# Kernel optimization log

Hardware: AMD Instinct MI355X
Metric: run time of the kernel (lower is better)

## Reference

```python
import jax, jax.numpy as jnp
import numpy as np

SOW_INIT = 1e-10  # sum_of_weights_initial_value
EPS = 1e-8       # torch.nn.CosineSimilarity default eps


def setup_inputs() -> dict:
    key = jax.random.key(0)
    k1, k2, k3 = jax.random.split(key, 3)
    input_image = jax.random.normal(k1, (1, 3, 224, 224), dtype=jnp.float32)
    masks = jax.random.uniform(k2, (1000, 224, 224), dtype=jnp.float32)
    # Linear encoder: flattened image [3*224*224] -> feature dim 128
    W = jax.random.normal(k3, (3, 224, 224, 128), dtype=jnp.float32) * 0.01
    return {"input_image": input_image, "masks": masks, "W": W}


def reference(input_image, masks, W):
    img = input_image[0]  # [3, H, W]
    # Encoder applied to (img * mask): rep_n = sum_chw (img*mask)[c,h,w] * W[c,h,w,f]
    # Precompute A[h,w,f] = sum_c img[c,h,w] * W[c,h,w,f] so masked reps never
    # materialize the [N,3,H,W] masked-image tensor.
    A = jnp.einsum('chw,chwf->hwf', img, W)          # [H, W, F]
    rep0 = jnp.sum(A, axis=(0, 1))                   # unmasked representation [F]
    reps = jnp.einsum('nhw,hwf->nf', masks, A)       # masked representations [N, F]

    # Cosine similarity (dim=1), clamped norms as in torch
    n0 = jnp.maximum(jnp.linalg.norm(rep0), EPS)
    nr = jnp.maximum(jnp.linalg.norm(reps, axis=1), EPS)
    sims = (reps @ rep0) / (nr * n0)                 # [N]

    H, Wd = masks.shape[1], masks.shape[2]
    imp0 = jnp.zeros((H, Wd), dtype=jnp.float32)
    unc0 = jnp.zeros((H, Wd), dtype=jnp.float32)
    sow0 = jnp.full((H, Wd), SOW_INIT, dtype=jnp.float32)

    def step(carry, inp):
        imp, unc, sow = carry
        m, s = inp  # mask [H,W], similarity scalar
        sow = sow + m
        prev = imp
        imp = imp + m * (s - imp) / sow
        unc = unc + (s - imp) * (s - prev) * m
        return (imp, unc, sow), None

    (imp, unc, sow), _ = jax.lax.scan(step, (imp0, unc0, sow0), (masks, sims))
    return jnp.stack([imp, unc, sow])  # [3, H, W]
```

## Files before the change

### kernel.cpp

```cpp
#include <hip/hip_runtime.h>
#include <hip/hip_bf16.h>
#include <stdint.h>

#define HWN 50176
#define NM  1000
#define FD  128
#define NSPLIT 98
#define KSTEPS 16
#define NSCAN 20
#define NPB 50

typedef __attribute__((ext_vector_type(8))) short short8;
typedef __attribute__((ext_vector_type(4))) float f32x4;

__device__ __forceinline__ unsigned short f2bf(float x) {
    union { float f; unsigned u; } v; v.f = x;
    unsigned r = v.u + 0x7FFFu + ((v.u >> 16) & 1u);
    return (unsigned short)(r >> 16);
}

#define AS1(p) ((const __attribute__((address_space(1))) unsigned int*)(p))
#define AS3(p) ((__attribute__((address_space(3))) unsigned int*)(p))

__global__ __launch_bounds__(256) void k_encode(const float* __restrict__ img,
                                                const float* __restrict__ Wt,
                                                unsigned short* __restrict__ Bpack,
                                                float* __restrict__ rep0part)
{
    const int t = threadIdx.x;
    const int f = t & 127;
    const int kt = blockIdx.x * 2 + (t >> 7);
    const int hw0 = kt * 32;
    float vals[32];
    float rsum = 0.f;
#pragma unroll
    for (int e = 0; e < 32; ++e) {
        const int hw = hw0 + e;
        float a = img[hw] * Wt[(size_t)hw * FD + f];
        a = fmaf(img[HWN + hw],     Wt[(size_t)(HWN + hw) * FD + f], a);
        a = fmaf(img[2 * HWN + hw], Wt[(size_t)(2 * HWN + hw) * FD + f], a);
        vals[e] = a;
        rsum += a;
    }
    char* tile = (char*)Bpack + (size_t)kt * 8192;
#pragma unroll
    for (int j = 0; j < 4; ++j) {
        short8 pk;
#pragma unroll
        for (int e = 0; e < 8; ++e) pk[e] = (short)f2bf(vals[j * 8 + e]);
        *reinterpret_cast<short8*>(tile + j * 2048 + (((f + j) & 127) << 4)) = pk;
    }
    __shared__ float red[256];
    red[t] = rsum;
    __syncthreads();
    if (t < 128) rep0part[(size_t)blockIdx.x * 128 + f] = red[t] + red[t + 128];
}

__global__ __launch_bounds__(256) void k_rep0red(const float* __restrict__ rep0part,
                                                 float* __restrict__ rep0)
{
    const int f = blockIdx.x;
    float s = 0.f;
    for (int b = threadIdx.x; b < 784; b += 256) s += rep0part[(size_t)b * 128 + f];
    __shared__ float red[256];
    red[threadIdx.x] = s;
    __syncthreads();
    for (int o = 128; o > 0; o >>= 1) {
        if (threadIdx.x < o) red[threadIdx.x] += red[threadIdx.x + o];
        __syncthreads();
    }
    if (threadIdx.x == 0) rep0[f] = red[0];
}

__global__ __launch_bounds__(512, 4) void k_gemm(const float* __restrict__ masks,
                                                 const unsigned short* __restrict__ Bpack,
                                                 float* __restrict__ partial)
{
    __shared__ __align__(16) char lds[3][24576];

    const int t = threadIdx.x;
    const int wv = t >> 6, lane = t & 63;
    const int lrow = lane & 15, kg = lane >> 4;
    const int mtile = blockIdx.x, split = blockIdx.y;
    const int n0 = mtile * 128;

    const int r0s = t >> 3, r1s = 64 + (t >> 3);
    const int c0 = (t & 7) ^ (r0s & 7);
    int arow0 = n0 + r0s; if (arow0 >= NM) arow0 = NM - 1;
    int arow1 = n0 + r1s; if (arow1 >= NM) arow1 = NM - 1;
    const float* aSrc0 = masks + (size_t)arow0 * HWN + split * 512 + c0 * 4;
    const float* aSrc1 = masks + (size_t)arow1 * HWN + split * 512 + c0 * 4;
    const char*  bSrc  = (const char*)Bpack + (size_t)split * (KSTEPS * 8192) + t * 16;

    const int r = wv * 16 + lrow;
    const int ao0 = r * 128 + (((2 * kg)     ^ (r & 7)) << 4);
    const int ao1 = r * 128 + ((((2 * kg)+1) ^ (r & 7)) << 4);
    int bo[8];
#pragma unroll
    for (int ft = 0; ft < 8; ++ft)
        bo[ft] = 16384 + kg * 2048 + (((ft * 16 + lrow + kg) & 127) << 4);

    f32x4 acc[8];
#pragma unroll
    for (int i = 0; i < 8; ++i) acc[i] = f32x4{0.f, 0.f, 0.f, 0.f};

#define STAGE(KS, BUF) do {                                                                              \
        char* b_ = &lds[BUF][0];                                                                         \
        __builtin_amdgcn_global_load_lds(AS1(aSrc0 + (KS) * 32), AS3(b_ + t * 16), 16, 0, 0);            \
        __builtin_amdgcn_global_load_lds(AS1(aSrc1 + (KS) * 32), AS3(b_ + 8192 + t * 16), 16, 0, 0);     \
        __builtin_amdgcn_global_load_lds(AS1(bSrc + (size_t)(KS) * 8192), AS3(b_ + 16384 + t * 16), 16, 0, 0); \
    } while (0)

    STAGE(0, 0);
    STAGE(1, 1);
    asm volatile("s_waitcnt vmcnt(3)" ::: "memory");
    __builtin_amdgcn_s_barrier();
    __builtin_amdgcn_sched_barrier(0);

    int cur = 0, stg = 2;
    for (int ks = 0; ks < KSTEPS; ++ks) {
        if (ks + 2 < KSTEPS) STAGE(ks + 2, stg);

        const char* A = &lds[cur][0];
        const f32x4 alo = *reinterpret_cast<const f32x4*>(A + ao0);
        const f32x4 ahi = *reinterpret_cast<const f32x4*>(A + ao1);
        union { short8 s; __hip_bfloat162 h[4]; } apk;
        apk.h[0] = __float22bfloat162_rn(float2{alo[0], alo[1]});
        apk.h[1] = __float22bfloat162_rn(float2{alo[2], alo[3]});
        apk.h[2] = __float22bfloat162_rn(float2{ahi[0], ahi[1]});
        apk.h[3] = __float22bfloat162_rn(float2{ahi[2], ahi[3]});
        short8 bfv[8];
#pragma unroll
        for (int ft = 0; ft < 8; ++ft)
            bfv[ft] = *reinterpret_cast<const short8*>(A + bo[ft]);

        asm volatile("s_waitcnt lgkmcnt(0)" ::: "memory");
        __builtin_amdgcn_sched_barrier(0);
        __builtin_amdgcn_s_setprio(1);
#pragma unroll
        for (int ft = 0; ft < 8; ++ft)
            acc[ft] = __builtin_amdgcn_mfma_f32_16x16x32_bf16(apk.s, bfv[ft], acc[ft], 0, 0, 0);
        __builtin_amdgcn_s_setprio(0);
        __builtin_amdgcn_sched_barrier(0);

        if (ks < KSTEPS - 2)       asm volatile("s_waitcnt vmcnt(3)" ::: "memory");
        else if (ks == KSTEPS - 2) asm volatile("s_waitcnt vmcnt(0)" ::: "memory");
        if (ks < KSTEPS - 1) {
            __builtin_amdgcn_s_barrier();
            __builtin_amdgcn_sched_barrier(0);
        }
        cur = (cur + 1 == 3) ? 0 : cur + 1;
        stg = (stg + 1 == 3) ? 0 : stg + 1;
    }
#undef STAGE

    const int crow = n0 + wv * 16 + (kg << 2);
    float* pb = partial + ((size_t)split * 1024 + crow) * FD + lrow;
#pragma unroll
    for (int ft = 0; ft < 8; ++ft)
#pragma unroll
        for (int rr = 0; rr < 4; ++rr)
            __builtin_nontemporal_store(acc[ft][rr], pb + (size_t)rr * FD + ft * 16);
}

__global__ __launch_bounds__(128) void k_sims(const float* __restrict__ partial,
                                              const float* __restrict__ rep0,
                                              float* __restrict__ sims)
{
    const int n = blockIdx.x;
    const int f = threadIdx.x;
    float rsum = 0.f;
    for (int s = 0; s < NSPLIT; ++s)
        rsum += __builtin_nontemporal_load(partial + ((size_t)s * 1024 + n) * FD + f);
    const float r0 = rep0[f];
    __shared__ float red0[128], red1[128], red2[128];
    red0[f] = rsum * r0;
    red1[f] = rsum * rsum;
    red2[f] = r0 * r0;
    __syncthreads();
    for (int o = 64; o > 0; o >>= 1) {
        if (f < o) {
            red0[f] += red0[f + o];
            red1[f] += red1[f + o];
            red2[f] += red2[f + o];
        }
        __syncthreads();
    }
    if (f == 0) {
        const float nr = fmaxf(sqrtf(red1[0]), 1e-8f);
        const float nz = fmaxf(sqrtf(red2[0]), 1e-8f);
        sims[n] = red0[0] / (nr * nz);
    }
}

__global__ __launch_bounds__(256) void k_colsums(const float* __restrict__ masks,
                                                 const float* __restrict__ sims,
                                                 float* __restrict__ Spart)
{
    __shared__ float s1v[NPB], s2v[NPB];
    const int t = threadIdx.x;
    const int split = blockIdx.y;
    if (t < NPB) {
        const float s = sims[split * NPB + t];
        s1v[t] = s;
        s2v[t] = s * s;
    }
    __syncthreads();
    const int pix = (blockIdx.x * 256 + t) * 4;
    const float* mp = masks + (size_t)split * NPB * HWN + pix;
    f32x4 s0 = {0.f,0.f,0.f,0.f}, s1 = s0, s2 = s0;
#pragma unroll 5
    for (int i = 0; i < NPB; ++i) {
        const f32x4 m = *reinterpret_cast<const f32x4*>(mp + (size_t)i * HWN);
        const float a = s1v[i], b = s2v[i];
        s0 += m;
#pragma unroll
        for (int e = 0; e < 4; ++e) {
            s1[e] = fmaf(m[e], a, s1[e]);
            s2[e] = fmaf(m[e], b, s2[e]);
        }
    }
    float* sp = Spart + (size_t)split * 3 * HWN + pix;
    __builtin_nontemporal_store(s0, reinterpret_cast<f32x4*>(sp));
    __builtin_nontemporal_store(s1, reinterpret_cast<f32x4*>(sp + HWN));
    __builtin_nontemporal_store(s2, reinterpret_cast<f32x4*>(sp + 2 * HWN));
}

__global__ __launch_bounds__(256) void k_final(const float* __restrict__ Spart,
                                               float* __restrict__ out)
{
    const int pix = (blockIdx.x * 256 + threadIdx.x) * 4;
    f32x4 s0 = {0.f,0.f,0.f,0.f}, s1 = s0, s2 = s0;
#pragma unroll 4
    for (int sp = 0; sp < NSCAN; ++sp) {
        const float* p = Spart + (size_t)sp * 3 * HWN + pix;
        s0 += __builtin_nontemporal_load(reinterpret_cast<const f32x4*>(p));
        s1 += __builtin_nontemporal_load(reinterpret_cast<const f32x4*>(p + HWN));
        s2 += __builtin_nontemporal_load(reinterpret_cast<const f32x4*>(p + 2 * HWN));
    }
    f32x4 imp, unc, sow;
#pragma unroll
    for (int e = 0; e < 4; ++e) {
        sow[e] = 1e-10f + s0[e];
        imp[e] = s1[e] / sow[e];
        unc[e] = fmaf(-imp[e], s1[e], s2[e]);
    }
    *reinterpret_cast<f32x4*>(out + pix) = imp;
    *reinterpret_cast<f32x4*>(out + HWN + pix) = unc;
    *reinterpret_cast<f32x4*>(out + 2 * HWN + pix) = sow;
}

extern "C" void kernel_launch(void* const* d_in, const int* in_sizes, int n_in,
                              void* d_out, int out_size, void* d_ws, size_t ws_size,
                              hipStream_t stream) {
    const float* img   = (const float*)d_in[0];
    const float* masks = (const float*)d_in[1];
    const float* Wt    = (const float*)d_in[2];
    float* out = (float*)d_out;

    char* ws = (char*)d_ws;
    unsigned short* Bpack = (unsigned short*)ws;
    float* partial  = (float*)(ws + 12845056);
    float* rep0part = partial;
    float* rep0     = (float*)(ws + 64225280);
    float* sims     = (float*)(ws + 64225792);
    float* Spart    = (float*)ws;

    hipLaunchKernelGGL(k_encode,  dim3(784), dim3(256), 0, stream, img, Wt, Bpack, rep0part);
    hipLaunchKernelGGL(k_rep0red, dim3(128), dim3(256), 0, stream, rep0part, rep0);
    hipLaunchKernelGGL(k_gemm,    dim3(8, NSPLIT), dim3(512), 0, stream, masks, Bpack, partial);
    hipLaunchKernelGGL(k_sims,    dim3(NM), dim3(128), 0, stream, partial, rep0, sims);
    hipLaunchKernelGGL(k_colsums, dim3(49, NSCAN), dim3(256), 0, stream, masks, sims, Spart);
    hipLaunchKernelGGL(k_final,   dim3(49), dim3(256), 0, stream, Spart, out);
}
```

Measured before the change: 141.1 us.

## Restructure mask GEMM: 4-wave blocks, 2 row-groups per wave, double buffering

```diff
diff --git a/kernel.cpp b/kernel.cpp
--- a/kernel.cpp
+++ b/kernel.cpp
@@ -48,7 +48,8 @@
         short8 pk;
 #pragma unroll
         for (int e = 0; e < 8; ++e) pk[e] = (short)f2bf(vals[j * 8 + e]);
-        *reinterpret_cast<short8*>(tile + j * 2048 + (((f + j) & 127) << 4)) = pk;
+        const int slot = (f * 4 + j) ^ ((f >> 1) & 3);
+        *reinterpret_cast<short8*>(tile + (slot << 4)) = pk;
     }
     __shared__ float red[256];
     red[t] = rsum;
@@ -72,95 +73,119 @@
     if (threadIdx.x == 0) rep0[f] = red[0];
 }
 
-__global__ __launch_bounds__(512, 4) void k_gemm(const float* __restrict__ masks,
+__global__ __launch_bounds__(256, 3) void k_gemm(const float* __restrict__ masks,
                                                  const unsigned short* __restrict__ Bpack,
                                                  float* __restrict__ partial)
 {
-    __shared__ __align__(16) char lds[3][24576];
+    __shared__ __align__(16) char lds[2][24576];
 
     const int t = threadIdx.x;
     const int wv = t >> 6, lane = t & 63;
     const int lrow = lane & 15, kg = lane >> 4;
-    const int mtile = blockIdx.x, split = blockIdx.y;
+
+    const int bid = blockIdx.x;
+    const int swz = (bid & 7) * 98 + (bid >> 3);
+    const int split = swz >> 3, mtile = swz & 7;
     const int n0 = mtile * 128;
 
-    const int r0s = t >> 3, r1s = 64 + (t >> 3);
-    const int c0 = (t & 7) ^ (r0s & 7);
-    int arow0 = n0 + r0s; if (arow0 >= NM) arow0 = NM - 1;
-    int arow1 = n0 + r1s; if (arow1 >= NM) arow1 = NM - 1;
-    const float* aSrc0 = masks + (size_t)arow0 * HWN + split * 512 + c0 * 4;
-    const float* aSrc1 = masks + (size_t)arow1 * HWN + split * 512 + c0 * 4;
-    const char*  bSrc  = (const char*)Bpack + (size_t)split * (KSTEPS * 8192) + t * 16;
-
-    const int r = wv * 16 + lrow;
-    const int ao0 = r * 128 + (((2 * kg)     ^ (r & 7)) << 4);
-    const int ao1 = r * 128 + ((((2 * kg)+1) ^ (r & 7)) << 4);
+    const int arow_l = t >> 3;
+    const int cA = (t & 7) ^ (arow_l & 7);
+    const float* aSrc[4];
+#pragma unroll
+    for (int o = 0; o < 4; ++o) {
+        int rowg = n0 + o * 32 + arow_l;
+        if (rowg >= NM) rowg = NM - 1;
+        aSrc[o] = masks + (size_t)rowg * HWN + split * 512 + cA * 4;
+    }
+    const char* bSrc = (const char*)Bpack + (size_t)split * (KSTEPS * 8192) + t * 16;
+
+    int ao[2][2];
+#pragma unroll
+    for (int g = 0; g < 2; ++g) {
+        const int r = wv * 32 + g * 16 + lrow;
+#pragma unroll
+        for (int w = 0; w < 2; ++w)
+            ao[g][w] = r * 128 + (((2 * kg + w) ^ (r & 7)) << 4);
+    }
     int bo[8];
 #pragma unroll
-    for (int ft = 0; ft < 8; ++ft)
-        bo[ft] = 16384 + kg * 2048 + (((ft * 16 + lrow + kg) & 127) << 4);
-
-    f32x4 acc[8];
-#pragma unroll
-    for (int i = 0; i < 8; ++i) acc[i] = f32x4{0.f, 0.f, 0.f, 0.f};
-
-#define STAGE(KS, BUF) do {                                                                              \
-        char* b_ = &lds[BUF][0];                                                                         \
-        __builtin_amdgcn_global_load_lds(AS1(aSrc0 + (KS) * 32), AS3(b_ + t * 16), 16, 0, 0);            \
-        __builtin_amdgcn_global_load_lds(AS1(aSrc1 + (KS) * 32), AS3(b_ + 8192 + t * 16), 16, 0, 0);     \
-        __builtin_amdgcn_global_load_lds(AS1(bSrc + (size_t)(KS) * 8192), AS3(b_ + 16384 + t * 16), 16, 0, 0); \
+    for (int ft = 0; ft < 8; ++ft) {
+        const int f = ft * 16 + lrow;
+        bo[ft] = 16384 + (((f * 4 + kg) ^ ((f >> 1) & 3)) << 4);
+    }
+
+    f32x4 acc[2][8];
+#pragma unroll
+    for (int g = 0; g < 2; ++g)
+#pragma unroll
+        for (int i = 0; i < 8; ++i) acc[g][i] = f32x4{0.f, 0.f, 0.f, 0.f};
+
+#define STAGE(KS, BUF) do {                                                                   \
+        char* b_ = &lds[BUF][0];                                                              \
+        __builtin_amdgcn_global_load_lds(AS1(aSrc[0] + (KS) * 32), AS3(b_ + t * 16), 16, 0, 0);          \
+        __builtin_amdgcn_global_load_lds(AS1(aSrc[1] + (KS) * 32), AS3(b_ + 4096  + t * 16), 16, 0, 0);  \
+        __builtin_amdgcn_global_load_lds(AS1(aSrc[2] + (KS) * 32), AS3(b_ + 8192  + t * 16), 16, 0, 0);  \
+        __builtin_amdgcn_global_load_lds(AS1(aSrc[3] + (KS) * 32), AS3(b_ + 12288 + t * 16), 16, 0, 0);  \
+        __builtin_amdgcn_global_load_lds(AS1(bSrc + (size_t)(KS) * 8192),        AS3(b_ + 16384 + t * 16), 16, 0, 0); \
+        __builtin_amdgcn_global_load_lds(AS1(bSrc + (size_t)(KS) * 8192 + 4096), AS3(b_ + 20480 + t * 16), 16, 0, 0); \
     } while (0)
 
     STAGE(0, 0);
-    STAGE(1, 1);
-    asm volatile("s_waitcnt vmcnt(3)" ::: "memory");
-    __builtin_amdgcn_s_barrier();
-    __builtin_amdgcn_sched_barrier(0);
-
-    int cur = 0, stg = 2;
+
     for (int ks = 0; ks < KSTEPS; ++ks) {
-        if (ks + 2 < KSTEPS) STAGE(ks + 2, stg);
-
-        const char* A = &lds[cur][0];
-        const f32x4 alo = *reinterpret_cast<const f32x4*>(A + ao0);
-        const f32x4 ahi = *reinterpret_cast<const f32x4*>(A + ao1);
-        union { short8 s; __hip_bfloat162 h[4]; } apk;
-        apk.h[0] = __float22bfloat162_rn(float2{alo[0], alo[1]});
-        apk.h[1] = __float22bfloat162_rn(float2{alo[2], alo[3]});
-        apk.h[2] = __float22bfloat162_rn(float2{ahi[0], ahi[1]});
-        apk.h[3] = __float22bfloat162_rn(float2{ahi[2], ahi[3]});
+        const int cur = ks & 1;
+        if (ks + 1 < KSTEPS) STAGE(ks + 1, cur ^ 1);
+        if (ks + 1 < KSTEPS) asm volatile("s_waitcnt vmcnt(6)" ::: "memory");
+        else                 asm volatile("s_waitcnt vmcnt(0)" ::: "memory");
+        __builtin_amdgcn_s_barrier();
+        __builtin_amdgcn_sched_barrier(0);
+
+        const char* B = &lds[cur][0];
         short8 bfv[8];
 #pragma unroll
         for (int ft = 0; ft < 8; ++ft)
-            bfv[ft] = *reinterpret_cast<const short8*>(A + bo[ft]);
+            bfv[ft] = *reinterpret_cast<const short8*>(B + bo[ft]);
+        f32x4 alo0 = *reinterpret_cast<const f32x4*>(B + ao[0][0]);
+        f32x4 ahi0 = *reinterpret_cast<const f32x4*>(B + ao[0][1]);
+        f32x4 alo1 = *reinterpret_cast<const f32x4*>(B + ao[1][0]);
+        f32x4 ahi1 = *reinterpret_cast<const f32x4*>(B + ao[1][1]);
+
+        union { short8 s; __hip_bfloat162 h[4]; } apk0, apk1;
+        apk0.h[0] = __float22bfloat162_rn(float2{alo0[0], alo0[1]});
+        apk0.h[1] = __float22bfloat162_rn(float2{alo0[2], alo0[3]});
+        apk0.h[2] = __float22bfloat162_rn(float2{ahi0[0], ahi0[1]});
+        apk0.h[3] = __float22bfloat162_rn(float2{ahi0[2], ahi0[3]});
+        apk1.h[0] = __float22bfloat162_rn(float2{alo1[0], alo1[1]});
+        apk1.h[1] = __float22bfloat162_rn(float2{alo1[2], alo1[3]});
+        apk1.h[2] = __float22bfloat162_rn(float2{ahi1[0], ahi1[1]});
+        apk1.h[3] = __float22bfloat162_rn(float2{ahi1[2], ahi1[3]});
 
         asm volatile("s_waitcnt lgkmcnt(0)" ::: "memory");
         __builtin_amdgcn_sched_barrier(0);
         __builtin_amdgcn_s_setprio(1);
 #pragma unroll
         for (int ft = 0; ft < 8; ++ft)
-            acc[ft] = __builtin_amdgcn_mfma_f32_16x16x32_bf16(apk.s, bfv[ft], acc[ft], 0, 0, 0);
+            acc[0][ft] = __builtin_amdgcn_mfma_f32_16x16x32_bf16(apk0.s, bfv[ft], acc[0][ft], 0, 0, 0);
+#pragma unroll
+        for (int ft = 0; ft < 8; ++ft)
+            acc[1][ft] = __builtin_amdgcn_mfma_f32_16x16x32_bf16(apk1.s, bfv[ft], acc[1][ft], 0, 0, 0);
         __builtin_amdgcn_s_setprio(0);
         __builtin_amdgcn_sched_barrier(0);
-
-        if (ks < KSTEPS - 2)       asm volatile("s_waitcnt vmcnt(3)" ::: "memory");
-        else if (ks == KSTEPS - 2) asm volatile("s_waitcnt vmcnt(0)" ::: "memory");
-        if (ks < KSTEPS - 1) {
-            __builtin_amdgcn_s_barrier();
-            __builtin_amdgcn_sched_barrier(0);
-        }
-        cur = (cur + 1 == 3) ? 0 : cur + 1;
-        stg = (stg + 1 == 3) ? 0 : stg + 1;
+        __builtin_amdgcn_s_barrier();
+        __builtin_amdgcn_sched_barrier(0);
     }
 #undef STAGE
 
-    const int crow = n0 + wv * 16 + (kg << 2);
-    float* pb = partial + ((size_t)split * 1024 + crow) * FD + lrow;
-#pragma unroll
-    for (int ft = 0; ft < 8; ++ft)
-#pragma unroll
-        for (int rr = 0; rr < 4; ++rr)
-            __builtin_nontemporal_store(acc[ft][rr], pb + (size_t)rr * FD + ft * 16);
+#pragma unroll
+    for (int g = 0; g < 2; ++g) {
+        const int crow = n0 + wv * 32 + g * 16 + (kg << 2);
+        float* pb = partial + ((size_t)split * 1024 + crow) * FD + lrow;
+#pragma unroll
+        for (int ft = 0; ft < 8; ++ft)
+#pragma unroll
+            for (int rr = 0; rr < 4; ++rr)
+                __builtin_nontemporal_store(acc[g][ft][rr], pb + (size_t)rr * FD + ft * 16);
+    }
 }
 
 __global__ __launch_bounds__(128) void k_sims(const float* __restrict__ partial,
@@ -268,7 +293,7 @@
 
     hipLaunchKernelGGL(k_encode,  dim3(784), dim3(256), 0, stream, img, Wt, Bpack, rep0part);
     hipLaunchKernelGGL(k_rep0red, dim3(128), dim3(256), 0, stream, rep0part, rep0);
-    hipLaunchKernelGGL(k_gemm,    dim3(8, NSPLIT), dim3(512), 0, stream, masks, Bpack, partial);
+    hipLaunchKernelGGL(k_gemm,    dim3(784), dim3(256), 0, stream, masks, Bpack, partial);
     hipLaunchKernelGGL(k_sims,    dim3(NM), dim3(128), 0, stream, partial, rep0, sims);
     hipLaunchKernelGGL(k_colsums, dim3(49, NSCAN), dim3(256), 0, stream, masks, sims, Spart);
     hipLaunchKernelGGL(k_final,   dim3(49), dim3(256), 0, stream, Spart, out);
```

Result: faster. 136.6 us (-3.2%).
